# Performance work log

Hardware: AMD Instinct MI355X
Metric: run time of the kernel (lower is better)

## Reference

```python
import jax, jax.numpy as jnp
import numpy as np

N = 65536      # batch rows
D = 32         # input_dim (number of per-feature sub-MLPs)
H = 128        # nodes_per_layer_in_sub_fn
# num_hidden_layers_per_feature_fn = 2 -> Linear(1,H),ReLU, Linear(H,H),ReLU, Linear(H,1)


def setup_inputs() -> dict:
    key = jax.random.key(0)
    ks = jax.random.split(key, 7)
    s1 = 1.0            # fan_in=1 kaiming-uniform-ish scale
    sH = 1.0 / np.sqrt(H)
    x = jax.random.normal(ks[0], (N, D), dtype=jnp.float32)
    W1 = jax.random.uniform(ks[1], (D, H), jnp.float32, -s1, s1)      # Linear(1,H) weight per feature
    b1 = jax.random.uniform(ks[2], (D, H), jnp.float32, -s1, s1)
    W2 = jax.random.uniform(ks[3], (D, H, H), jnp.float32, -sH, sH)   # Linear(H,H) per feature
    b2 = jax.random.uniform(ks[4], (D, H), jnp.float32, -sH, sH)
    W3 = jax.random.uniform(ks[5], (D, H), jnp.float32, -sH, sH)      # Linear(H,1) per feature
    b3 = jax.random.uniform(ks[6], (D,), jnp.float32, -sH, sH)
    return {"x": x, "W1": W1, "b1": b1, "W2": W2, "b2": b2, "W3": W3, "b3": b3}


def reference(x, W1, b1, W2, b2, W3, b3):
    # h1[n,d,h] = relu(x[n,d] * W1[d,h] + b1[d,h])
    h1 = jax.nn.relu(x[:, :, None] * W1[None, :, :] + b1[None, :, :])          # [N,D,H]
    # h2: per-feature batched GEMM, Linear(H,H) + ReLU
    h2 = jax.nn.relu(jnp.einsum('ndh,dhk->ndk', h1, W2) + b2[None, :, :])      # [N,D,H]
    # per-feature output Linear(H,1), then sum across features, keepdim
    per_feat = jnp.einsum('ndh,dh->nd', h2, W3) + b3[None, :]                  # [N,D]
    return jnp.sum(per_feat, axis=1, keepdims=True)                            # [N,1]
```

## Files before the change

kernel.cpp:

```cpp
#include <hip/hip_runtime.h>
#include <hip/hip_bf16.h>
#include <stdint.h>


#define D_FEAT 32
#define H_DIM  128
#define SLOTS  16
#define THREADS 256
#define NTILE  64

typedef float    f32x16 __attribute__((ext_vector_type(16)));
typedef short    bf16x8 __attribute__((ext_vector_type(8)));
typedef uint32_t u32;

static __device__ __forceinline__ u32 cvtpk(float lo, float hi) {
    u32 r;
    asm("v_cvt_pk_bf16_f32 %0, %1, %2" : "=v"(r) : "v"(lo), "v"(hi));
    return r;
}
static __device__ __forceinline__ bf16x8 frag4(u32 a, u32 b, u32 c, u32 d) {
    int4 t = make_int4((int)a, (int)b, (int)c, (int)d);
    return __builtin_bit_cast(bf16x8, t);
}
static __device__ __forceinline__ bf16x8 frag1(u32 a) { return frag4(a, 0u, 0u, 0u); }

#define MFMA32(A, B, C) __builtin_amdgcn_mfma_f32_32x32x16_bf16((A), (B), (C), 0, 0, 0)

static __device__ __forceinline__ bf16x8 relu_pack(const f32x16& v, int s) {
    u32 c0 = cvtpk(fmaxf(v[8*s+0], 0.f), fmaxf(v[8*s+1], 0.f));
    u32 c1 = cvtpk(fmaxf(v[8*s+2], 0.f), fmaxf(v[8*s+3], 0.f));
    u32 c2 = cvtpk(fmaxf(v[8*s+4], 0.f), fmaxf(v[8*s+5], 0.f));
    u32 c3 = cvtpk(fmaxf(v[8*s+6], 0.f), fmaxf(v[8*s+7], 0.f));
    return frag4(c0, c1, c2, c3);
}

static __device__ __forceinline__ float epi(const f32x16& a0, const f32x16& a1,
                                            const float* __restrict__ W3s,
                                            int mo0, int mo1, int g) {
    float p[4];
#pragma unroll
    for (int q = 0; q < 4; ++q) {
        const float4 wa = *reinterpret_cast<const float4*>(&W3s[32 * mo0 + 4 * g + 8 * q]);
        const float4 wb = *reinterpret_cast<const float4*>(&W3s[32 * mo1 + 4 * g + 8 * q]);
        float t;
        t = fmaxf(a0[4*q+0], 0.f) * wa.x;
        t = fmaf(fmaxf(a0[4*q+1], 0.f), wa.y, t);
        t = fmaf(fmaxf(a0[4*q+2], 0.f), wa.z, t);
        t = fmaf(fmaxf(a0[4*q+3], 0.f), wa.w, t);
        t = fmaf(fmaxf(a1[4*q+0], 0.f), wb.x, t);
        t = fmaf(fmaxf(a1[4*q+1], 0.f), wb.y, t);
        t = fmaf(fmaxf(a1[4*q+2], 0.f), wb.z, t);
        t = fmaf(fmaxf(a1[4*q+3], 0.f), wb.w, t);
        p[q] = t;
    }
    return (p[0] + p[1]) + (p[2] + p[3]);
}

__global__ __launch_bounds__(THREADS, 2) void kan_main(
    const float* __restrict__ x,
    const float* __restrict__ W1,
    const float* __restrict__ b1,
    const float* __restrict__ W2,
    const float* __restrict__ b2,
    const float* __restrict__ W3,
    const float* __restrict__ b3,
    float* __restrict__ out)
{
    __shared__ float xall[NTILE * 64];
    __shared__ float W3s[H_DIM];

    const int tid   = threadIdx.x;
    const int d     = blockIdx.x / SLOTS;
    const int bslot = blockIdx.x % SLOTS;
    const int w     = tid >> 6;
    const int wm    = w >> 1;
    const int wn    = w & 1;
    const int l     = tid & 63;
    const int l31   = l & 31;
    const int g     = l >> 5;

#pragma unroll
    for (int i = 0; i < (NTILE * 64) / THREADS; ++i) {
        int idx = tid + THREADS * i;
        int tl  = idx >> 6;
        xall[idx] = x[(size_t)((bslot + SLOTS * tl) * 64 + (idx & 63)) * D_FEAT + d];
    }
    if (tid < H_DIM) W3s[tid] = W3[d * H_DIM + tid];

    float b3s = 0.f;
#pragma unroll
    for (int k = 0; k < D_FEAT; ++k) b3s += b3[k];

    const int mo0 = 2 * wm, mo1 = 2 * wm + 1;
    u32 w1b1[4], b2w[2];
#pragma unroll
    for (int mt = 0; mt < 4; ++mt) {
        int m = 32 * mt + l31;
        u32 v = cvtpk(W1[d * H_DIM + m], b1[d * H_DIM + m]);
        w1b1[mt] = g ? 0u : v;
    }
    b2w[0] = g ? 0u : cvtpk(b2[d * H_DIM + 32 * mo0 + l31], 0.f);
    b2w[1] = g ? 0u : cvtpk(b2[d * H_DIM + 32 * mo1 + l31], 0.f);
    const bf16x8 onesB = frag1(g ? 0u : 0x00003F80u);

    bf16x8 w2f[2][8];
    {
        const float* W2d = W2 + (size_t)d * H_DIM * H_DIM;
#pragma unroll
        for (int j = 0; j < 2; ++j) {
            int mm = 32 * (mo0 + j) + l31;
#pragma unroll
            for (int ks = 0; ks < 8; ++ks) {
                u32 dw[4];
#pragma unroll
                for (int p = 0; p < 4; ++p) {
                    int e0 = 2 * p, e1 = 2 * p + 1;
                    int k0 = 16 * ks + 4 * g + (e0 & 3) + 8 * (e0 >> 2);
                    int k1 = 16 * ks + 4 * g + (e1 & 3) + 8 * (e1 >> 2);
                    dw[p] = cvtpk(W2d[(size_t)k0 * H_DIM + mm],
                                  W2d[(size_t)k1 * H_DIM + mm]);
                }
                w2f[j][ks] = frag4(dw[0], dw[1], dw[2], dw[3]);
            }
        }
    }
    __syncthreads();

    const f32x16 zc = {};
    const bool addb3 = (d == 0) && (wm == 0);

    for (int ip = 0; ip < NTILE; ip += 2) {
        const int rb0 = (bslot + SLOTS * (ip + 0)) * 64 + 32 * wn;
        const int rb1 = (bslot + SLOTS * (ip + 1)) * 64 + 32 * wn;
        float xv0 = xall[(ip + 0) * 64 + 32 * wn + l31];
        float xv1 = xall[(ip + 1) * 64 + 32 * wn + l31];
        bf16x8 Bx0 = frag1(g ? 0u : cvtpk(xv0, 1.0f));
        bf16x8 Bx1 = frag1(g ? 0u : cvtpk(xv1, 1.0f));

        f32x16 a00 = MFMA32(frag1(b2w[0]), onesB, zc);
        f32x16 a01 = MFMA32(frag1(b2w[1]), onesB, zc);
        f32x16 a10 = MFMA32(frag1(b2w[0]), onesB, zc);
        f32x16 a11 = MFMA32(frag1(b2w[1]), onesB, zc);

#pragma unroll
        for (int mt = 0; mt < 4; ++mt) {
            f32x16 d10 = MFMA32(frag1(w1b1[mt]), Bx0, zc);
            f32x16 d11 = MFMA32(frag1(w1b1[mt]), Bx1, zc);
            bf16x8 bl0 = relu_pack(d10, 0), bh0 = relu_pack(d10, 1);
            bf16x8 bl1 = relu_pack(d11, 0), bh1 = relu_pack(d11, 1);
            a00 = MFMA32(w2f[0][2 * mt + 0], bl0, a00);
            a10 = MFMA32(w2f[0][2 * mt + 0], bl1, a10);
            a01 = MFMA32(w2f[1][2 * mt + 0], bl0, a01);
            a11 = MFMA32(w2f[1][2 * mt + 0], bl1, a11);
            a00 = MFMA32(w2f[0][2 * mt + 1], bh0, a00);
            a10 = MFMA32(w2f[0][2 * mt + 1], bh1, a10);
            a01 = MFMA32(w2f[1][2 * mt + 1], bh0, a01);
            a11 = MFMA32(w2f[1][2 * mt + 1], bh1, a11);
        }

        float rs0 = epi(a00, a01, W3s, mo0, mo1, g);
        float rs1 = epi(a10, a11, W3s, mo0, mo1, g);
        rs0 += __shfl_xor(rs0, 32, 64);
        rs1 += __shfl_xor(rs1, 32, 64);
        if (addb3) { rs0 += b3s; rs1 += b3s; }
        if (!g) {
            atomicAdd(&out[rb0 + l31], rs0);
            atomicAdd(&out[rb1 + l31], rs1);
        }
    }
}

extern "C" void kernel_launch(void* const* d_in, const int* in_sizes, int n_in,
                              void* d_out, int out_size, void* d_ws, size_t ws_size,
                              hipStream_t stream) {
    const float* x  = (const float*)d_in[0];
    const float* W1 = (const float*)d_in[1];
    const float* b1 = (const float*)d_in[2];
    const float* W2 = (const float*)d_in[3];
    const float* b2 = (const float*)d_in[4];
    const float* W3 = (const float*)d_in[5];
    const float* b3 = (const float*)d_in[6];
    float* out = (float*)d_out;
    const int N = in_sizes[0] / D_FEAT;

    hipMemsetAsync(out, 0, (size_t)N * sizeof(float), stream);
    kan_main<<<D_FEAT * SLOTS, THREADS, 0, stream>>>(x, W1, b1, W2, b2, W3, b3, out);
}
```

Baseline: 160.4 us.

## Replace global atomics with per-feature workspace partials and a separate reduction kernel

When enough workspace is available, each block writes its per-feature, per-half partial sums into a 64xN scratch buffer with plain stores, and a second kernel sums the 64 partials per row and adds the b3 bias. This is meant to remove the contention and serialization of 32-way float atomicAdd on every output element, along with the memset. It also staggers each block's row slot by feature index so concurrent blocks touch different rows. The cost is about 16 MB of extra scratch traffic and an extra kernel launch. The atomic path is kept as a fallback when the workspace is too small.

Measured after the change: 178.0 us. 1.11x slower.

```diff
diff --git a/kernel.cpp b/kernel.cpp
--- a/kernel.cpp
+++ b/kernel.cpp
@@ -5,6 +5,7 @@
 
 #define D_FEAT 32
 #define H_DIM  128
+#define N_TOT  65536
 #define SLOTS  16
 #define THREADS 256
 #define NTILE  64
@@ -56,6 +57,7 @@
     return (p[0] + p[1]) + (p[2] + p[3]);
 }
 
+template <int USE_WS>
 __global__ __launch_bounds__(THREADS, 2) void kan_main(
     const float* __restrict__ x,
     const float* __restrict__ W1,
@@ -64,7 +66,7 @@
     const float* __restrict__ b2,
     const float* __restrict__ W3,
     const float* __restrict__ b3,
-    float* __restrict__ out)
+    float* __restrict__ dst)
 {
     __shared__ float xall[NTILE * 64];
     __shared__ float W3s[H_DIM];
@@ -72,6 +74,7 @@
     const int tid   = threadIdx.x;
     const int d     = blockIdx.x / SLOTS;
     const int bslot = blockIdx.x % SLOTS;
+    const int eslot = (bslot + d) & (SLOTS - 1);
     const int w     = tid >> 6;
     const int wm    = w >> 1;
     const int wn    = w & 1;
@@ -83,13 +86,15 @@
     for (int i = 0; i < (NTILE * 64) / THREADS; ++i) {
         int idx = tid + THREADS * i;
         int tl  = idx >> 6;
-        xall[idx] = x[(size_t)((bslot + SLOTS * tl) * 64 + (idx & 63)) * D_FEAT + d];
+        xall[idx] = x[(size_t)((eslot + SLOTS * tl) * 64 + (idx & 63)) * D_FEAT + d];
     }
     if (tid < H_DIM) W3s[tid] = W3[d * H_DIM + tid];
 
     float b3s = 0.f;
-#pragma unroll
-    for (int k = 0; k < D_FEAT; ++k) b3s += b3[k];
+    if (USE_WS == 0) {
+#pragma unroll
+        for (int k = 0; k < D_FEAT; ++k) b3s += b3[k];
+    }
 
     const int mo0 = 2 * wm, mo1 = 2 * wm + 1;
     u32 w1b1[4], b2w[2];
@@ -127,11 +132,14 @@
     __syncthreads();
 
     const f32x16 zc = {};
-    const bool addb3 = (d == 0) && (wm == 0);
-
-    for (int ip = 0; ip < NTILE; ip += 2) {
-        const int rb0 = (bslot + SLOTS * (ip + 0)) * 64 + 32 * wn;
-        const int rb1 = (bslot + SLOTS * (ip + 1)) * 64 + 32 * wn;
+    const bool addb3 = (USE_WS == 0) && (d == 0) && (wm == 0);
+    const int ipoff = (USE_WS == 0 && (d & 16)) ? (NTILE / 2) : 0;
+    float* const wsbase = dst + (size_t)(2 * d + wm) * N_TOT;
+
+    for (int ii = 0; ii < NTILE; ii += 2) {
+        const int ip = (ii + ipoff) & (NTILE - 1);
+        const int rb0 = (eslot + SLOTS * (ip + 0)) * 64 + 32 * wn;
+        const int rb1 = (eslot + SLOTS * (ip + 1)) * 64 + 32 * wn;
         float xv0 = xall[(ip + 0) * 64 + 32 * wn + l31];
         float xv1 = xall[(ip + 1) * 64 + 32 * wn + l31];
         bf16x8 Bx0 = frag1(g ? 0u : cvtpk(xv0, 1.0f));
@@ -162,12 +170,37 @@
         float rs1 = epi(a10, a11, W3s, mo0, mo1, g);
         rs0 += __shfl_xor(rs0, 32, 64);
         rs1 += __shfl_xor(rs1, 32, 64);
-        if (addb3) { rs0 += b3s; rs1 += b3s; }
-        if (!g) {
-            atomicAdd(&out[rb0 + l31], rs0);
-            atomicAdd(&out[rb1 + l31], rs1);
+        if (USE_WS) {
+            if (!g) {
+                wsbase[rb0 + l31] = rs0;
+                wsbase[rb1 + l31] = rs1;
+            }
+        } else {
+            if (addb3) { rs0 += b3s; rs1 += b3s; }
+            if (!g) {
+                atomicAdd(&dst[rb0 + l31], rs0);
+                atomicAdd(&dst[rb1 + l31], rs1);
+            }
         }
     }
+}
+
+__global__ __launch_bounds__(256) void kan_reduce(const float* __restrict__ ws,
+                                                  const float* __restrict__ b3,
+                                                  float* __restrict__ out) {
+    int n = blockIdx.x * blockDim.x + threadIdx.x;
+    float b3s = 0.f;
+#pragma unroll
+    for (int k = 0; k < D_FEAT; ++k) b3s += b3[k];
+    float s0 = 0.f, s1 = 0.f, s2 = 0.f, s3 = 0.f;
+#pragma unroll
+    for (int j = 0; j < 64; j += 4) {
+        s0 += ws[(size_t)(j + 0) * N_TOT + n];
+        s1 += ws[(size_t)(j + 1) * N_TOT + n];
+        s2 += ws[(size_t)(j + 2) * N_TOT + n];
+        s3 += ws[(size_t)(j + 3) * N_TOT + n];
+    }
+    out[n] = ((s0 + s1) + (s2 + s3)) + b3s;
 }
 
 extern "C" void kernel_launch(void* const* d_in, const int* in_sizes, int n_in,
@@ -181,8 +214,14 @@
     const float* W3 = (const float*)d_in[5];
     const float* b3 = (const float*)d_in[6];
     float* out = (float*)d_out;
-    const int N = in_sizes[0] / D_FEAT;
-
-    hipMemsetAsync(out, 0, (size_t)N * sizeof(float), stream);
-    kan_main<<<D_FEAT * SLOTS, THREADS, 0, stream>>>(x, W1, b1, W2, b2, W3, b3, out);
-}
+
+    const size_t ws_need = (size_t)64 * N_TOT * sizeof(float);
+    if (ws_size >= ws_need) {
+        float* ws = (float*)d_ws;
+        kan_main<1><<<D_FEAT * SLOTS, THREADS, 0, stream>>>(x, W1, b1, W2, b2, W3, b3, ws);
+        kan_reduce<<<N_TOT / 256, 256, 0, stream>>>(ws, b3, out);
+    } else {
+        hipMemsetAsync(out, 0, (size_t)N_TOT * sizeof(float), stream);
+        kan_main<0><<<D_FEAT * SLOTS, THREADS, 0, stream>>>(x, W1, b1, W2, b2, W3, b3, out);
+    }
+}
```
